# Kernel tuning notes

Measured on AMD Instinct MI355X. Metric: run time of the kernel, lower is better.

Reference implementation:

```python
import jax, jax.numpy as jnp
import numpy as np

NUM_HEADS = 12

def _get_rel_pos(q_size, k_size, rel_pos):
    # rel_pos already has shape (2*max(q,k)-1, head_dim) -> no resize needed
    q_coords = jnp.arange(q_size)[:, None] * max(k_size / q_size, 1.0)
    k_coords = jnp.arange(k_size)[None, :] * max(q_size / k_size, 1.0)
    rel = (q_coords - k_coords + (k_size - 1) * max(q_size / k_size, 1.0)).astype(jnp.int32)
    return rel_pos[rel.reshape(-1)].reshape(q_size, k_size, -1)  # (q, k, head_dim)


def setup_inputs() -> dict:
    key = jax.random.key(0)
    ks = jax.random.split(key, 7)
    B, H, W, C = 1, 64, 64, 768
    head_dim = C // NUM_HEADS
    return {
        "x": jax.random.normal(ks[0], (B, H, W, C), jnp.float32),
        "qkv_w": jax.random.normal(ks[1], (C, 3 * C), jnp.float32) * 0.02,
        "qkv_b": jax.random.normal(ks[2], (3 * C,), jnp.float32) * 0.02,
        "rel_pos_h": jax.random.normal(ks[3], (2 * H - 1, head_dim), jnp.float32) * 0.02,
        "rel_pos_w": jax.random.normal(ks[4], (2 * W - 1, head_dim), jnp.float32) * 0.02,
        "proj_w": jax.random.normal(ks[5], (C, C), jnp.float32) * 0.02,
        "proj_b": jax.random.normal(ks[6], (C,), jnp.float32) * 0.02,
    }


def reference(x, qkv_w, qkv_b, rel_pos_h, rel_pos_w, proj_w, proj_b):
    B, H, W, C = x.shape
    nh = NUM_HEADS
    hd = C // nh
    scale = hd ** (-0.5)
    S = H * W

    qkv = x @ qkv_w + qkv_b                              # (B,H,W,3C)
    qkv = qkv.reshape(B, S, 3, nh, hd).transpose(2, 0, 3, 1, 4).reshape(3, B * nh, S, hd)
    q, k, v = qkv[0], qkv[1], qkv[2]                     # (B*nh, S, hd)

    attn = jnp.einsum('bqd,bkd->bqk', q * scale, k)      # (B*nh, S, S)

    rh = _get_rel_pos(H, H, rel_pos_h)                   # (H,H,hd)
    rw = _get_rel_pos(W, W, rel_pos_w)                   # (W,W,hd)
    r_q = q.reshape(B * nh, H, W, hd)
    rel_h = jnp.einsum('bhwc,hkc->bhwk', r_q, rh)        # (B*nh,H,W,H)
    rel_w = jnp.einsum('bhwc,wkc->bhwk', r_q, rw)        # (B*nh,H,W,W)
    attn = (attn.reshape(B * nh, H, W, H, W)
            + rel_h[:, :, :, :, None]
            + rel_w[:, :, :, None, :]).reshape(B * nh, S, S)

    attn = jax.nn.softmax(attn, axis=-1)
    out = jnp.einsum('bqk,bkd->bqd', attn, v)            # (B*nh, S, hd)
    out = out.reshape(B, nh, H, W, hd).transpose(0, 2, 3, 1, 4).reshape(B, H, W, C)
    return out @ proj_w + proj_b
```

## Files before the change

### kernel.cpp

```cpp
#include <hip/hip_runtime.h>
#include <hip/hip_bf16.h>

#define S_TOK 4096
#define CDIM  768
#define N3C   2304
#define NH    12
#define HD    64

#define LOG2E 1.44269504f

typedef __attribute__((ext_vector_type(8))) short short8;
typedef __attribute__((ext_vector_type(4))) short short4v;
typedef __attribute__((ext_vector_type(4))) float float4v;
typedef __attribute__((ext_vector_type(4))) unsigned uint4v;

__device__ __forceinline__ float b2f(short s) {
    return __uint_as_float(((unsigned)(unsigned short)s) << 16);
}
__device__ __forceinline__ short f2b(float f) {
    unsigned u = __float_as_uint(f);
    unsigned r = (u + 0x7FFFu + ((u >> 16) & 1u)) >> 16;
    return (short)r;
}

#if __has_builtin(__builtin_amdgcn_exp2f)
#define EXP2F __builtin_amdgcn_exp2f
#else
#define EXP2F exp2f
#endif

__device__ __forceinline__ unsigned pack_trunc(float a, float b) {
    return __builtin_amdgcn_perm(__float_as_uint(b), __float_as_uint(a), 0x07060302u);
}

__device__ __forceinline__ short8 u4_to_s8(unsigned a, unsigned b, unsigned c, unsigned d) {
    union { uint4v u; short8 s; } t;
    t.u = (uint4v){a, b, c, d};
    return t.s;
}

__device__ __forceinline__ void load_lds16(const void* g, void* l) {
    __builtin_amdgcn_global_load_lds(
        (const __attribute__((address_space(1))) unsigned int*)g,
        (__attribute__((address_space(3))) unsigned int*)l, 16, 0, 0);
}

__global__ __launch_bounds__(256) void cast_bf16_kernel(
    const float* __restrict__ in, short* __restrict__ out, int n4)
{
    int i = blockIdx.x * 256 + threadIdx.x;
    if (i >= n4) return;
    float4 v = ((const float4*)in)[i];
    short4v o4 = { f2b(v.x), f2b(v.y), f2b(v.z), f2b(v.w) };
    *(short4v*)&out[(size_t)i * 4] = o4;
}

__global__ __launch_bounds__(256) void transpose_cast_kernel(
    const float* __restrict__ in, short* __restrict__ out, int R, int C)
{
    __shared__ float t[64][65];
    const int tid = threadIdx.x;
    const int c0 = blockIdx.x * 64, r0 = blockIdx.y * 64;
    const int li = tid >> 6;
    const int lj = tid & 63;
#pragma unroll
    for (int p = 0; p < 16; ++p) {
        int i = p * 4 + li;
        t[i][lj] = in[(size_t)(r0 + i) * C + c0 + lj];
    }
    __syncthreads();
#pragma unroll
    for (int p = 0; p < 16; ++p) {
        int i = p * 4 + li;
        out[(size_t)(c0 + i) * R + r0 + lj] = f2b(t[lj][i]);
    }
}

#define GEMM_CORE(A_, Bt_)                                                     \
    __shared__ __align__(16) short a_s[128][64];                               \
    __shared__ __align__(16) short b_s[128][64];                               \
    const int tid  = threadIdx.x;                                              \
    const int m0 = blockIdx.y * 128;                                           \
    const int n0 = blockIdx.x * 128;                                           \
    const int lane = tid & 63, w = tid >> 6;                                   \
    const int l15 = lane & 15, quad = lane >> 4;                               \
    const int wr = w >> 1, wc = w & 1;                                         \
    const int roff0 = (quad ^ (l15 & 7)) << 4;                                 \
    const int roff1 = roff0 ^ 64;                                              \
    const int srow0 = w * 8 + (lane >> 3);                                     \
    const int sslot = (lane & 7) ^ ((lane >> 3) & 7);                          \
    const short* ga = A_ + (size_t)(m0 + srow0) * 768 + sslot * 8;             \
    const short* gb = Bt_ + (size_t)(n0 + srow0) * 768 + sslot * 8;            \
    short* la = &a_s[w * 8][0];                                                \
    short* lb = &b_s[w * 8][0];                                                \
    float4v acc[4][4];                                                         \
    _Pragma("unroll")                                                          \
    for (int i = 0; i < 4; ++i)                                                \
        _Pragma("unroll")                                                      \
        for (int j = 0; j < 4; ++j) acc[i][j] = (float4v){0.f,0.f,0.f,0.f};    \
    for (int k0 = 0; k0 < 768; k0 += 64) {                                     \
        __syncthreads();                                                       \
        _Pragma("unroll")                                                      \
        for (int i = 0; i < 4; ++i) {                                          \
            load_lds16(ga + (size_t)i * (32 * 768) + k0, la + i * 32 * 64);    \
            load_lds16(gb + (size_t)i * (32 * 768) + k0, lb + i * 32 * 64);    \
        }                                                                      \
        __syncthreads();                                                       \
        _Pragma("unroll")                                                      \
        for (int kk = 0; kk < 64; kk += 32) {                                  \
            const int roff = kk ? roff1 : roff0;                               \
            short8 af[4], bfr[4];                                              \
            _Pragma("unroll")                                                  \
            for (int i = 0; i < 4; ++i)                                        \
                af[i] = *(const short8*)((const char*)&a_s[wr*64 + i*16 + l15][0] + roff); \
            _Pragma("unroll")                                                  \
            for (int j = 0; j < 4; ++j)                                        \
                bfr[j] = *(const short8*)((const char*)&b_s[wc*64 + j*16 + l15][0] + roff); \
            _Pragma("unroll")                                                  \
            for (int i = 0; i < 4; ++i)                                        \
                _Pragma("unroll")                                              \
                for (int j = 0; j < 4; ++j)                                    \
                    acc[i][j] = __builtin_amdgcn_mfma_f32_16x16x32_bf16(       \
                        af[i], bfr[j], acc[i][j], 0, 0, 0);                    \
        }                                                                      \
    }

__global__ __launch_bounds__(256) void gemm_qkv_mfma(
    const short* __restrict__ A, const short* __restrict__ Bt,
    const float* __restrict__ bias,
    short* __restrict__ Qb, short* __restrict__ Kb, short* __restrict__ Vt)
{
    GEMM_CORE(A, Bt)

    const int sec = n0 / CDIM;
    float bj[4];
#pragma unroll
    for (int j = 0; j < 4; ++j) bj[j] = bias[n0 + wc*64 + j*16 + l15];

    if (sec < 2) {
        short* dst = (sec == 0) ? Qb : Kb;
#pragma unroll
        for (int i = 0; i < 4; ++i)
#pragma unroll
            for (int j = 0; j < 4; ++j) {
                const int nn = (n0 + wc*64 + j*16 + l15) % CDIM;
                const int head = nn >> 6, d = nn & 63;
#pragma unroll
                for (int r = 0; r < 4; ++r) {
                    const int s = m0 + wr*64 + i*16 + quad*4 + r;
                    dst[((size_t)head * S_TOK + s) * HD + d] = f2b(acc[i][j][r] + bj[j]);
                }
            }
    } else {
#pragma unroll
        for (int i = 0; i < 4; ++i)
#pragma unroll
            for (int j = 0; j < 4; ++j) {
                const int nn = (n0 + wc*64 + j*16 + l15) % CDIM;
                const int head = nn >> 6, d = nn & 63;
                const int sbase = m0 + wr*64 + i*16 + quad*4;
                short4v v4;
#pragma unroll
                for (int r = 0; r < 4; ++r) v4[r] = f2b(acc[i][j][r] + bj[j]);
                *(short4v*)&Vt[((size_t)head * HD + d) * S_TOK + sbase] = v4;
            }
    }
}

__global__ __launch_bounds__(256) void gemm_proj_mfma(
    const short* __restrict__ A, const short* __restrict__ Bt,
    const float* __restrict__ bias, float* __restrict__ out)
{
    GEMM_CORE(A, Bt)

    float bj[4];
#pragma unroll
    for (int j = 0; j < 4; ++j) bj[j] = bias[n0 + wc*64 + j*16 + l15];

#pragma unroll
    for (int i = 0; i < 4; ++i)
#pragma unroll
        for (int j = 0; j < 4; ++j) {
            const int n = n0 + wc*64 + j*16 + l15;
#pragma unroll
            for (int r = 0; r < 4; ++r) {
                const int s = m0 + wr*64 + i*16 + quad*4 + r;
                out[(size_t)s * CDIM + n] = acc[i][j][r] + bj[j];
            }
        }
}

__global__ __launch_bounds__(256) void rel_mfma_kernel(
    const short* __restrict__ Qb, const float* __restrict__ rph,
    const float* __restrict__ rpw, short* __restrict__ RelhT,
    short* __restrict__ Relw)
{
    __shared__ __align__(16) short q_s [64][72];
    __shared__ __align__(16) short rh_s[64][72];
    __shared__ __align__(16) short rw_s[128][72];

    const int tid  = threadIdx.x;
    const int y    = blockIdx.x;
    const int head = blockIdx.y;
    const int s0   = y * 64;
    const int w = tid >> 6, lane = tid & 63;
    const int l15 = lane & 15, quad = lane >> 4;
    const int srow = tid >> 2;
    const int scol = (tid & 3) << 4;

    {
        const uint4* g = (const uint4*)(Qb + ((size_t)head * S_TOK + s0 + srow) * HD + scol);
        *(uint4*)&q_s[srow][scol]     = g[0];
        *(uint4*)&q_s[srow][scol + 8] = g[1];
    }
    {
        const float* g = rph + (size_t)(y + srow) * HD + scol;
        short tmp[16];
#pragma unroll
        for (int i = 0; i < 16; i += 4) {
            float4 v = *(const float4*)(g + i);
            tmp[i] = f2b(v.x); tmp[i+1] = f2b(v.y); tmp[i+2] = f2b(v.z); tmp[i+3] = f2b(v.w);
        }
        *(short8*)&rh_s[srow][scol]     = *(short8*)&tmp[0];
        *(short8*)&rh_s[srow][scol + 8] = *(short8*)&tmp[8];
    }
#pragma unroll
    for (int half = 0; half < 2; ++half) {
        const int row = srow + half * 64;
        const int rr  = row > 126 ? 126 : row;
        const float* g = rpw + (size_t)rr * HD + scol;
        short tmp[16];
#pragma unroll
        for (int i = 0; i < 16; i += 4) {
            float4 v = *(const float4*)(g + i);
            tmp[i] = f2b(v.x); tmp[i+1] = f2b(v.y); tmp[i+2] = f2b(v.z); tmp[i+3] = f2b(v.w);
        }
        *(short8*)&rw_s[row][scol]     = *(short8*)&tmp[0];
        *(short8*)&rw_s[row][scol + 8] = *(short8*)&tmp[8];
    }
    __syncthreads();

    const short8 qa0 = *(const short8*)&q_s[w * 16 + l15][quad * 8];
    const short8 qa1 = *(const short8*)&q_s[w * 16 + l15][32 + quad * 8];

#pragma unroll
    for (int ct = 0; ct < 4; ++ct) {
        const int jj = ct * 16 + l15;
        short8 b0 = *(const short8*)&rh_s[jj][quad * 8];
        short8 b1 = *(const short8*)&rh_s[jj][32 + quad * 8];
        float4v z = (float4v){0.f, 0.f, 0.f, 0.f};
        z = __builtin_amdgcn_mfma_f32_16x16x32_bf16(qa0, b0, z, 0, 0, 0);
        z = __builtin_amdgcn_mfma_f32_16x16x32_bf16(qa1, b1, z, 0, 0, 0);
        const int ky = 63 - jj;
        short4v o4;
#pragma unroll
        for (int r = 0; r < 4; ++r) o4[r] = f2b(z[r] * LOG2E);
        *(short4v*)&RelhT[((size_t)head * HD + ky) * S_TOK + s0 + w * 16 + quad * 4] = o4;
    }

#pragma unroll
    for (int ct = 0; ct < 8; ++ct) {
        const int j = ct * 16 + l15;
        short8 b0 = *(const short8*)&rw_s[j][quad * 8];
        short8 b1 = *(const short8*)&rw_s[j][32 + quad * 8];
        float4v z = (float4v){0.f, 0.f, 0.f, 0.f};
        z = __builtin_amdgcn_mfma_f32_16x16x32_bf16(qa0, b0, z, 0, 0, 0);
        z = __builtin_amdgcn_mfma_f32_16x16x32_bf16(qa1, b1, z, 0, 0, 0);
#pragma unroll
        for (int r = 0; r < 4; ++r) {
            const int q  = w * 16 + quad * 4 + r;
            const int kx = q + 63 - j;
            if (kx >= 0 && kx < 64)
                Relw[((size_t)head * S_TOK + s0 + q) * HD + kx] = f2b(z[r] * LOG2E);
        }
    }
}

__global__ __launch_bounds__(256, 3) void flash_kernel(
    const short* __restrict__ Qb, const short* __restrict__ Kb,
    const short* __restrict__ Vt, const short* __restrict__ RelhT,
    const short* __restrict__ Relw, short* __restrict__ attn_b)
{
    __shared__ __align__(16) short lds_s[24576];

    const int tid  = threadIdx.x;
    const int head = blockIdx.y;
    const int s0   = blockIdx.x * 64;
    const int w    = tid >> 6, lane = tid & 63;
    const int l15  = lane & 15, quad = lane >> 4;
    const int ph   = w >> 1;
    const int qh   = w & 1;

    const float C1 = 0.125f * LOG2E;

    const int lj = lane >> 3;
    const int sl = (lane & 7) ^ lj;
    const int kf0 = (lj & 3) + ((lj & 4) << 1) + qh * 32;

    const short* pKs = Kb + (size_t)head * S_TOK * HD
                     + (size_t)(ph * 32 * 64 + kf0) * HD + sl * 8;
    const short* pVs = Vt + ((size_t)head * HD + qh * 32 + lj) * S_TOK
                     + ph * 32 * 64 + sl * 8;

    short* lk0 = &lds_s[(ph * 2 + 0) << 12] + qh * 32 * 64;
    short* lk1 = &lds_s[(ph * 2 + 1) << 12] + qh * 32 * 64;
    short* lv  = &lds_s[16384 + (ph << 12)] + qh * 32 * 64;
    const short* krd0 = &lds_s[(ph * 2 + 0) << 12];
    const short* krd1 = &lds_s[(ph * 2 + 1) << 12];
    const short* vrd  = &lds_s[16384 + (ph << 12)];

    const int roff0 = (quad ^ (l15 & 7)) << 4;
    const int roff1 = roff0 ^ 64;

    short8 qb[2][2];
#pragma unroll
    for (int qt = 0; qt < 2; ++qt) {
        const short* qrow = Qb + ((size_t)head * S_TOK + s0 + qh * 32 + qt * 16 + l15) * HD;
        qb[qt][0] = *(const short8*)(qrow + quad * 8);
        qb[qt][1] = *(const short8*)(qrow + 32 + quad * 8);
    }

    float rwv[2][4][4];
#pragma unroll
    for (int qt = 0; qt < 2; ++qt) {
        const short* rwrow = Relw + ((size_t)head * S_TOK + s0 + qh * 32 + qt * 16 + l15) * HD;
#pragma unroll
        for (int kt = 0; kt < 4; ++kt) {
            const int base = ((kt & 1) << 2) | ((kt >> 1) << 5);
            short4v v = *(const short4v*)(rwrow + base + quad * 8);
#pragma unroll
            for (int r = 0; r < 4; ++r) rwv[qt][kt][r] = b2f(v[r]);
        }
    }

    const short* rhbase = RelhT + (size_t)head * HD * S_TOK + s0 + qh * 32 + l15;
    float rhc0 = b2f(rhbase[(size_t)(ph * 32) * S_TOK]);
    float rhc1 = b2f(rhbase[(size_t)(ph * 32) * S_TOK + 16]);

    short8 aones;
#pragma unroll
    for (int j = 0; j < 8; ++j) aones[j] = (short)0x3F80;

    float4v od[2][4];
#pragma unroll
    for (int qt = 0; qt < 2; ++qt)
#pragma unroll
        for (int dt = 0; dt < 4; ++dt) od[qt][dt] = (float4v){0.f, 0.f, 0.f, 0.f};
    float4v dq0 = (float4v){0.f, 0.f, 0.f, 0.f};
    float4v dq1 = (float4v){0.f, 0.f, 0.f, 0.f};

    load_lds16(pKs,        lk0);
    load_lds16(pKs + 1024, lk0 + 8  * 64);
    load_lds16(pKs + 256,  lk0 + 16 * 64);
    load_lds16(pKs + 1280, lk0 + 24 * 64);
    __syncthreads();

    for (int t = 0; t < 32; ++t) {
        const int cur = t & 1;
        const short* krd = cur ? krd1 : krd0;
        short* lkn = cur ? lk0 : lk1;

        load_lds16(pVs,               lv);
        load_lds16(pVs + 8  * S_TOK,  lv + 8  * 64);
        load_lds16(pVs + 16 * S_TOK,  lv + 16 * 64);
        load_lds16(pVs + 24 * S_TOK,  lv + 24 * 64);
        if (t < 31) {
            const short* pk = pKs + 4096;
            load_lds16(pk,        lkn);
            load_lds16(pk + 1024, lkn + 8  * 64);
            load_lds16(pk + 256,  lkn + 16 * 64);
            load_lds16(pk + 1280, lkn + 24 * 64);
        }
        pKs += 4096;
        pVs += 64;

        short rhn0, rhn1;
        if (t < 31) {
            rhn0 = rhbase[(size_t)(ph * 32 + t + 1) * S_TOK];
            rhn1 = rhbase[(size_t)(ph * 32 + t + 1) * S_TOK + 16];
        }

        unsigned pkk[2][8];
#pragma unroll
        for (int kt = 0; kt < 4; ++kt) {
            const char* krp = (const char*)(krd + (kt * 16 + l15) * 64);
            const short8 ka0 = *(const short8*)(krp + roff0);
            const short8 ka1 = *(const short8*)(krp + roff1);
            {
                float4v z = (float4v){0.f, 0.f, 0.f, 0.f};
                z = __builtin_amdgcn_mfma_f32_16x16x32_bf16(ka0, qb[0][0], z, 0, 0, 0);
                z = __builtin_amdgcn_mfma_f32_16x16x32_bf16(ka1, qb[0][1], z, 0, 0, 0);
                float p0 = EXP2F(C1 * z[0] + (rhc0 + rwv[0][kt][0]));
                float p1 = EXP2F(C1 * z[1] + (rhc0 + rwv[0][kt][1]));
                float p2 = EXP2F(C1 * z[2] + (rhc0 + rwv[0][kt][2]));
                float p3 = EXP2F(C1 * z[3] + (rhc0 + rwv[0][kt][3]));
                pkk[0][kt * 2]     = pack_trunc(p0, p1);
                pkk[0][kt * 2 + 1] = pack_trunc(p2, p3);
            }
            {
                float4v z = (float4v){0.f, 0.f, 0.f, 0.f};
                z = __builtin_amdgcn_mfma_f32_16x16x32_bf16(ka0, qb[1][0], z, 0, 0, 0);
                z = __builtin_amdgcn_mfma_f32_16x16x32_bf16(ka1, qb[1][1], z, 0, 0, 0);
                float p0 = EXP2F(C1 * z[0] + (rhc1 + rwv[1][kt][0]));
                float p1 = EXP2F(C1 * z[1] + (rhc1 + rwv[1][kt][1]));
                float p2 = EXP2F(C1 * z[2] + (rhc1 + rwv[1][kt][2]));
                float p3 = EXP2F(C1 * z[3] + (rhc1 + rwv[1][kt][3]));
                pkk[1][kt * 2]     = pack_trunc(p0, p1);
                pkk[1][kt * 2 + 1] = pack_trunc(p2, p3);
            }
        }
        const short8 pb00 = u4_to_s8(pkk[0][0], pkk[0][1], pkk[0][2], pkk[0][3]);
        const short8 pb01 = u4_to_s8(pkk[0][4], pkk[0][5], pkk[0][6], pkk[0][7]);
        const short8 pb10 = u4_to_s8(pkk[1][0], pkk[1][1], pkk[1][2], pkk[1][3]);
        const short8 pb11 = u4_to_s8(pkk[1][4], pkk[1][5], pkk[1][6], pkk[1][7]);

        __syncthreads();

        __builtin_amdgcn_s_setprio(1);
#pragma unroll
        for (int dt = 0; dt < 4; ++dt) {
            const char* vrp = (const char*)(vrd + (dt * 16 + l15) * 64);
            const short8 va0 = *(const short8*)(vrp + roff0);
            const short8 va1 = *(const short8*)(vrp + roff1);
            od[0][dt] = __builtin_amdgcn_mfma_f32_16x16x32_bf16(va0, pb00, od[0][dt], 0, 0, 0);
            od[0][dt] = __builtin_amdgcn_mfma_f32_16x16x32_bf16(va1, pb01, od[0][dt], 0, 0, 0);
            od[1][dt] = __builtin_amdgcn_mfma_f32_16x16x32_bf16(va0, pb10, od[1][dt], 0, 0, 0);
            od[1][dt] = __builtin_amdgcn_mfma_f32_16x16x32_bf16(va1, pb11, od[1][dt], 0, 0, 0);
        }
        dq0 = __builtin_amdgcn_mfma_f32_16x16x32_bf16(aones, pb00, dq0, 0, 0, 0);
        dq0 = __builtin_amdgcn_mfma_f32_16x16x32_bf16(aones, pb01, dq0, 0, 0, 0);
        dq1 = __builtin_amdgcn_mfma_f32_16x16x32_bf16(aones, pb10, dq1, 0, 0, 0);
        dq1 = __builtin_amdgcn_mfma_f32_16x16x32_bf16(aones, pb11, dq1, 0, 0, 0);
        __builtin_amdgcn_s_setprio(0);

        if (t < 31) {
            rhc0 = b2f(rhn0);
            rhc1 = b2f(rhn1);
        }
        __syncthreads();
    }

    float* cf = (float*)lds_s;
    if (ph == 1) {
#pragma unroll
        for (int qt = 0; qt < 2; ++qt)
#pragma unroll
            for (int dt = 0; dt < 4; ++dt) {
                float* dst = &cf[((((qh * 2 + qt) * 4 + dt) * 16) + quad * 4) * 16 + l15];
#pragma unroll
                for (int r = 0; r < 4; ++r) dst[r * 16] = od[qt][dt][r];
            }
        if (quad == 0) {
            cf[4096 + (qh * 2 + 0) * 16 + l15] = dq0[0];
            cf[4096 + (qh * 2 + 1) * 16 + l15] = dq1[0];
        }
    }
    __syncthreads();
    if (ph == 0) {
#pragma unroll
        for (int qt = 0; qt < 2; ++qt) {
            const float dtot = ((qt == 0) ? dq0[0] : dq1[0])
                             + cf[4096 + (qh * 2 + qt) * 16 + l15];
            const float inv = 1.f / dtot;
            short* outp = attn_b + (size_t)(s0 + qh * 32 + qt * 16 + l15) * CDIM + head * HD;
#pragma unroll
            for (int dt = 0; dt < 4; ++dt) {
                const float* src = &cf[((((qh * 2 + qt) * 4 + dt) * 16) + quad * 4) * 16 + l15];
                short4v o4;
#pragma unroll
                for (int r = 0; r < 4; ++r)
                    o4[r] = f2b((od[qt][dt][r] + src[r * 16]) * inv);
                *(short4v*)(outp + dt * 16 + quad * 4) = o4;
            }
        }
    }
}

extern "C" void kernel_launch(void* const* d_in, const int* in_sizes, int n_in,
                              void* d_out, int out_size, void* d_ws, size_t ws_size,
                              hipStream_t stream)
{
    const float* x    = (const float*)d_in[0];
    const float* qkvw = (const float*)d_in[1];
    const float* qkvb = (const float*)d_in[2];
    const float* rph  = (const float*)d_in[3];
    const float* rpw  = (const float*)d_in[4];
    const float* pw   = (const float*)d_in[5];
    const float* pb   = (const float*)d_in[6];
    float* out = (float*)d_out;

    const size_t HSD = (size_t)NH * S_TOK * HD;
    short* xb     = (short*)d_ws;
    short* wt     = xb + (size_t)S_TOK * CDIM;
    short* pwt    = wt + (size_t)N3C * CDIM;
    short* Qb     = pwt + (size_t)CDIM * CDIM;
    short* Kb     = Qb + HSD;
    short* Vt     = Kb + HSD;
    short* RelhT  = Vt + HSD;
    short* Relw   = RelhT + HSD;
    short* attn_b = Relw + HSD;

    cast_bf16_kernel<<<S_TOK * CDIM / 4 / 256, 256, 0, stream>>>(x, xb, S_TOK * CDIM / 4);
    transpose_cast_kernel<<<dim3(N3C / 64, CDIM / 64), 256, 0, stream>>>(qkvw, wt, CDIM, N3C);
    transpose_cast_kernel<<<dim3(CDIM / 64, CDIM / 64), 256, 0, stream>>>(pw, pwt, CDIM, CDIM);

    gemm_qkv_mfma<<<dim3(N3C / 128, S_TOK / 128), 256, 0, stream>>>(
        xb, wt, qkvb, Qb, Kb, Vt);
    rel_mfma_kernel<<<dim3(64, NH), 256, 0, stream>>>(Qb, rph, rpw, RelhT, Relw);
    flash_kernel<<<dim3(64, NH), 256, 0, stream>>>(Qb, Kb, Vt, RelhT, Relw, attn_b);
    gemm_proj_mfma<<<dim3(CDIM / 128, S_TOK / 128), 256, 0, stream>>>(
        attn_b, pwt, pb, out);
}
```

Measured before the change: 209.6 us.

## Double-buffer V in flash loop and stage GEMM epilogues through LDS

The flash kernel now double-buffers the V tiles alongside K, prefetching both one iteration ahead, which removes one barrier per iteration. LDS grows to 64KB and occupancy drops from 3 to 2 blocks per CU. The QKV and projection GEMM epilogues now stage results through shared memory so global writes become coalesced 16-byte stores instead of scattered 2- or 4-byte ones. The extra syncs in the epilogues and the lower flash occupancy are the tradeoffs.

```diff
diff --git a/kernel.cpp b/kernel.cpp
--- a/kernel.cpp
+++ b/kernel.cpp
@@ -77,8 +77,9 @@
 }
 
 #define GEMM_CORE(A_, Bt_)                                                     \
-    __shared__ __align__(16) short a_s[128][64];                               \
-    __shared__ __align__(16) short b_s[128][64];                               \
+    __shared__ __align__(16) short smem[2][128][64];                           \
+    auto a_s = smem[0];                                                        \
+    auto b_s = smem[1];                                                        \
     const int tid  = threadIdx.x;                                              \
     const int m0 = blockIdx.y * 128;                                           \
     const int n0 = blockIdx.x * 128;                                           \
@@ -138,32 +139,57 @@
     for (int j = 0; j < 4; ++j) bj[j] = bias[n0 + wc*64 + j*16 + l15];
 
     if (sec < 2) {
-        short* dst = (sec == 0) ? Qb : Kb;
-#pragma unroll
-        for (int i = 0; i < 4; ++i)
-#pragma unroll
-            for (int j = 0; j < 4; ++j) {
-                const int nn = (n0 + wc*64 + j*16 + l15) % CDIM;
-                const int head = nn >> 6, d = nn & 63;
-#pragma unroll
-                for (int r = 0; r < 4; ++r) {
-                    const int s = m0 + wr*64 + i*16 + quad*4 + r;
-                    dst[((size_t)head * S_TOK + s) * HD + d] = f2b(acc[i][j][r] + bj[j]);
-                }
-            }
+        short* base = (sec == 0) ? Qb : Kb;
+        short (*tile)[68] = (short(*)[68])&smem[0][0][0];
+#pragma unroll
+        for (int h = 0; h < 2; ++h) {
+            __syncthreads();
+            if (wc == h) {
+#pragma unroll
+                for (int i = 0; i < 4; ++i)
+#pragma unroll
+                    for (int j = 0; j < 4; ++j)
+#pragma unroll
+                        for (int r = 0; r < 4; ++r)
+                            tile[wr*64 + i*16 + quad*4 + r][j*16 + l15] =
+                                f2b(acc[i][j][r] + bj[j]);
+            }
+            __syncthreads();
+            const int nn = (n0 % CDIM) + h * 64;
+            const int head = nn >> 6;
+            short* dst = base + ((size_t)head * S_TOK + m0) * HD;
+#pragma unroll
+            for (int it = 0; it < 4; ++it) {
+                const int row = it * 32 + (tid >> 3), c = (tid & 7) * 8;
+                *(short8*)&dst[(size_t)row * HD + c] = *(const short8*)&tile[row][c];
+            }
+        }
     } else {
-#pragma unroll
-        for (int i = 0; i < 4; ++i)
-#pragma unroll
-            for (int j = 0; j < 4; ++j) {
-                const int nn = (n0 + wc*64 + j*16 + l15) % CDIM;
-                const int head = nn >> 6, d = nn & 63;
-                const int sbase = m0 + wr*64 + i*16 + quad*4;
-                short4v v4;
-#pragma unroll
-                for (int r = 0; r < 4; ++r) v4[r] = f2b(acc[i][j][r] + bj[j]);
-                *(short4v*)&Vt[((size_t)head * HD + d) * S_TOK + sbase] = v4;
-            }
+        short (*tv)[130] = (short(*)[130])&smem[0][0][0];
+#pragma unroll
+        for (int h = 0; h < 2; ++h) {
+            __syncthreads();
+            if (wc == h) {
+#pragma unroll
+                for (int i = 0; i < 4; ++i)
+#pragma unroll
+                    for (int j = 0; j < 4; ++j) {
+                        short4v v4;
+#pragma unroll
+                        for (int r = 0; r < 4; ++r) v4[r] = f2b(acc[i][j][r] + bj[j]);
+                        *(short4v*)&tv[j*16 + l15][wr*64 + i*16 + quad*4] = v4;
+                    }
+            }
+            __syncthreads();
+            const int nn = (n0 % CDIM) + h * 64;
+            const int head = nn >> 6;
+            short* dst = Vt + (size_t)head * HD * S_TOK + m0;
+#pragma unroll
+            for (int it = 0; it < 4; ++it) {
+                const int nr = it * 16 + (tid >> 4), sc = (tid & 15) * 8;
+                *(short8*)&dst[(size_t)nr * S_TOK + sc] = *(const short8*)&tv[nr][sc];
+            }
+        }
     }
 }
 
@@ -177,17 +203,36 @@
 #pragma unroll
     for (int j = 0; j < 4; ++j) bj[j] = bias[n0 + wc*64 + j*16 + l15];
 
-#pragma unroll
-    for (int i = 0; i < 4; ++i)
-#pragma unroll
-        for (int j = 0; j < 4; ++j) {
-            const int n = n0 + wc*64 + j*16 + l15;
-#pragma unroll
-            for (int r = 0; r < 4; ++r) {
-                const int s = m0 + wr*64 + i*16 + quad*4 + r;
-                out[(size_t)s * CDIM + n] = acc[i][j][r] + bj[j];
-            }
-        }
+    float* tf = (float*)&smem[0][0][0];
+#pragma unroll
+    for (int h = 0; h < 2; ++h) {
+        __syncthreads();
+        if (wr == h) {
+#pragma unroll
+            for (int i = 0; i < 4; ++i)
+#pragma unroll
+                for (int j = 0; j < 4; ++j) {
+                    const int cc = wc*16 + j*4 + (l15 >> 2);
+                    const int ci = l15 & 3;
+#pragma unroll
+                    for (int r = 0; r < 4; ++r) {
+                        const int row = i*16 + quad*4 + r;
+                        const int pc = cc ^ ((row & 7) << 2);
+                        tf[row * 128 + pc * 4 + ci] = acc[i][j][r] + bj[j];
+                    }
+                }
+        }
+        __syncthreads();
+        float* dst = out + (size_t)(m0 + h * 64) * CDIM + n0;
+#pragma unroll
+        for (int it = 0; it < 8; ++it) {
+            const int row = it * 8 + (tid >> 5);
+            const int gc = tid & 31;
+            const int pc = gc ^ ((row & 7) << 2);
+            float4 v = *(const float4*)&tf[row * 128 + pc * 4];
+            *(float4*)&dst[(size_t)row * CDIM + gc * 4] = v;
+        }
+    }
 }
 
 __global__ __launch_bounds__(256) void rel_mfma_kernel(
@@ -276,12 +321,12 @@
     }
 }
 
-__global__ __launch_bounds__(256, 3) void flash_kernel(
+__global__ __launch_bounds__(256, 2) void flash_kernel(
     const short* __restrict__ Qb, const short* __restrict__ Kb,
     const short* __restrict__ Vt, const short* __restrict__ RelhT,
     const short* __restrict__ Relw, short* __restrict__ attn_b)
 {
-    __shared__ __align__(16) short lds_s[24576];
+    __shared__ __align__(16) short lds_s[32768];
 
     const int tid  = threadIdx.x;
     const int head = blockIdx.y;
@@ -297,17 +342,18 @@
     const int sl = (lane & 7) ^ lj;
     const int kf0 = (lj & 3) + ((lj & 4) << 1) + qh * 32;
 
-    const short* pKs = Kb + (size_t)head * S_TOK * HD
+    const short* pK0 = Kb + (size_t)head * S_TOK * HD
                      + (size_t)(ph * 32 * 64 + kf0) * HD + sl * 8;
-    const short* pVs = Vt + ((size_t)head * HD + qh * 32 + lj) * S_TOK
+    const short* pV0 = Vt + ((size_t)head * HD + qh * 32 + lj) * S_TOK
                      + ph * 32 * 64 + sl * 8;
 
-    short* lk0 = &lds_s[(ph * 2 + 0) << 12] + qh * 32 * 64;
-    short* lk1 = &lds_s[(ph * 2 + 1) << 12] + qh * 32 * 64;
-    short* lv  = &lds_s[16384 + (ph << 12)] + qh * 32 * 64;
-    const short* krd0 = &lds_s[(ph * 2 + 0) << 12];
-    const short* krd1 = &lds_s[(ph * 2 + 1) << 12];
-    const short* vrd  = &lds_s[16384 + (ph << 12)];
+    short* lk[2]  = { &lds_s[(ph*2 + 0) << 12] + qh*32*64,
+                      &lds_s[(ph*2 + 1) << 12] + qh*32*64 };
+    short* lv[2]  = { &lds_s[16384 + ((ph*2 + 0) << 12)] + qh*32*64,
+                      &lds_s[16384 + ((ph*2 + 1) << 12)] + qh*32*64 };
+    const short* krd[2] = { &lds_s[(ph*2 + 0) << 12], &lds_s[(ph*2 + 1) << 12] };
+    const short* vrd[2] = { &lds_s[16384 + ((ph*2 + 0) << 12)],
+                            &lds_s[16384 + ((ph*2 + 1) << 12)] };
 
     const int roff0 = (quad ^ (l15 & 7)) << 4;
     const int roff1 = roff0 ^ 64;
@@ -349,41 +395,42 @@
     float4v dq0 = (float4v){0.f, 0.f, 0.f, 0.f};
     float4v dq1 = (float4v){0.f, 0.f, 0.f, 0.f};
 
-    load_lds16(pKs,        lk0);
-    load_lds16(pKs + 1024, lk0 + 8  * 64);
-    load_lds16(pKs + 256,  lk0 + 16 * 64);
-    load_lds16(pKs + 1280, lk0 + 24 * 64);
+    load_lds16(pK0,        lk[0]);
+    load_lds16(pK0 + 1024, lk[0] + 8  * 64);
+    load_lds16(pK0 + 256,  lk[0] + 16 * 64);
+    load_lds16(pK0 + 1280, lk[0] + 24 * 64);
+    load_lds16(pV0,               lv[0]);
+    load_lds16(pV0 + 8  * S_TOK,  lv[0] + 8  * 64);
+    load_lds16(pV0 + 16 * S_TOK,  lv[0] + 16 * 64);
+    load_lds16(pV0 + 24 * S_TOK,  lv[0] + 24 * 64);
     __syncthreads();
 
     for (int t = 0; t < 32; ++t) {
         const int cur = t & 1;
-        const short* krd = cur ? krd1 : krd0;
-        short* lkn = cur ? lk0 : lk1;
-
-        load_lds16(pVs,               lv);
-        load_lds16(pVs + 8  * S_TOK,  lv + 8  * 64);
-        load_lds16(pVs + 16 * S_TOK,  lv + 16 * 64);
-        load_lds16(pVs + 24 * S_TOK,  lv + 24 * 64);
-        if (t < 31) {
-            const short* pk = pKs + 4096;
-            load_lds16(pk,        lkn);
-            load_lds16(pk + 1024, lkn + 8  * 64);
-            load_lds16(pk + 256,  lkn + 16 * 64);
-            load_lds16(pk + 1280, lkn + 24 * 64);
-        }
-        pKs += 4096;
-        pVs += 64;
 
         short rhn0, rhn1;
         if (t < 31) {
+            const short* gk = pK0 + (size_t)(t + 1) * 4096;
+            const short* gv = pV0 + (t + 1) * 64;
+            short* k1 = lk[cur ^ 1];
+            short* v1 = lv[cur ^ 1];
+            load_lds16(gk,        k1);
+            load_lds16(gk + 1024, k1 + 8  * 64);
+            load_lds16(gk + 256,  k1 + 16 * 64);
+            load_lds16(gk + 1280, k1 + 24 * 64);
+            load_lds16(gv,              v1);
+            load_lds16(gv + 8  * S_TOK, v1 + 8  * 64);
+            load_lds16(gv + 16 * S_TOK, v1 + 16 * 64);
+            load_lds16(gv + 24 * S_TOK, v1 + 24 * 64);
             rhn0 = rhbase[(size_t)(ph * 32 + t + 1) * S_TOK];
             rhn1 = rhbase[(size_t)(ph * 32 + t + 1) * S_TOK + 16];
         }
 
+        const short* kc = krd[cur];
         unsigned pkk[2][8];
 #pragma unroll
         for (int kt = 0; kt < 4; ++kt) {
-            const char* krp = (const char*)(krd + (kt * 16 + l15) * 64);
+            const char* krp = (const char*)(kc + (kt * 16 + l15) * 64);
             const short8 ka0 = *(const short8*)(krp + roff0);
             const short8 ka1 = *(const short8*)(krp + roff1);
             {
@@ -414,12 +461,11 @@
         const short8 pb10 = u4_to_s8(pkk[1][0], pkk[1][1], pkk[1][2], pkk[1][3]);
         const short8 pb11 = u4_to_s8(pkk[1][4], pkk[1][5], pkk[1][6], pkk[1][7]);
 
-        __syncthreads();
-
+        const short* vc = vrd[cur];
         __builtin_amdgcn_s_setprio(1);
 #pragma unroll
         for (int dt = 0; dt < 4; ++dt) {
-            const char* vrp = (const char*)(vrd + (dt * 16 + l15) * 64);
+            const char* vrp = (const char*)(vc + (dt * 16 + l15) * 64);
             const short8 va0 = *(const short8*)(vrp + roff0);
             const short8 va1 = *(const short8*)(vrp + roff1);
             od[0][dt] = __builtin_amdgcn_mfma_f32_16x16x32_bf16(va0, pb00, od[0][dt], 0, 0, 0);
```

After: 240.4 us. +14.7%, slower.
